# Kernel tuning notes

Hardware: AMD Instinct MI355X
Metric: run time of the kernel (lower is better)

## Reference

```python
import jax, jax.numpy as jnp
import numpy as np

B, D, U = 8192, 2048, 2048  # batch rows, input dim, units
NB_FACTOR = 3
MASK_DENSITY = 1.0 / 16.0  # butterfly-like sparse factor density


def _glorot_uniform(key, shape):
    fan_in, fan_out = shape[0], shape[-1]
    limit = np.sqrt(6.0 / (fan_in + fan_out)).astype(np.float32)
    return jax.random.uniform(key, shape, jnp.float32, -limit, limit)


def setup_inputs() -> dict:
    key = jax.random.key(0)
    kx, km0, km1, km2, kk0, kk1, kk2, ks = jax.random.split(key, 8)
    x = jax.random.normal(kx, (B, D), jnp.float32)
    # Fixed sparsity patterns (constants, like K.constant sparsity_masks)
    m0 = (jax.random.uniform(km0, (D, U)) < MASK_DENSITY).astype(jnp.float32)
    m1 = (jax.random.uniform(km1, (U, U)) < MASK_DENSITY).astype(jnp.float32)
    m2 = (jax.random.uniform(km2, (U, U)) < MASK_DENSITY).astype(jnp.float32)
    k0 = _glorot_uniform(kk0, (D, U))
    k1 = _glorot_uniform(kk1, (U, U))
    k2 = _glorot_uniform(kk2, (U, U))
    scaling = _glorot_uniform(ks, (1,))  # scaler weight, shape (1,)
    bias = jnp.zeros((U,), jnp.float32)
    return {"x": x, "k0": k0, "k1": k1, "k2": k2,
            "m0": m0, "m1": m1, "m2": m2,
            "scaling": scaling, "bias": bias}


def reference(x, k0, k1, k2, m0, m1, m2, scaling, bias):
    # output = activation(scaling * (x @ (k0*m0) @ (k1*m1) @ (k2*m2)) + bias)
    out = x @ (k0 * m0)          # [B, U]
    out = out @ (k1 * m1)        # [B, U]
    out = out @ (k2 * m2)        # [B, U]
    out = scaling * out + bias   # scale then channels-last bias add
    return jax.nn.relu(out)
```

## Files before the change

kernel.cpp:

```cpp
#include <hip/hip_runtime.h>
#include <hip/hip_bf16.h>


typedef __attribute__((ext_vector_type(8))) short  short8;
typedef __attribute__((ext_vector_type(8))) ushort ushort8v;
typedef __attribute__((ext_vector_type(4))) float  f32x4;

#define KD 2048
#define ND 2048

__device__ __forceinline__ ushort f2b(float f) {
    union { float f; unsigned u; } v; v.f = f;
    unsigned r = v.u + 0x7fffu + ((v.u >> 16) & 1u);
    return (ushort)(r >> 16);
}

__device__ __forceinline__ void gload16(const ushort* g, ushort* l) {
    __builtin_amdgcn_global_load_lds(
        (const __attribute__((address_space(1))) void*)g,
        (__attribute__((address_space(3))) void*)l, 16, 0, 0);
}

__global__ __launch_bounds__(256)
void convx(const float* __restrict__ x, ushort* __restrict__ xb)
{
    const size_t i = (size_t)blockIdx.x * 256 + threadIdx.x;
    const float4* src = reinterpret_cast<const float4*>(x) + i * 2;
    const float4 f0 = src[0], f1 = src[1];
    ushort8v u;
    u[0]=f2b(f0.x); u[1]=f2b(f0.y); u[2]=f2b(f0.z); u[3]=f2b(f0.w);
    u[4]=f2b(f1.x); u[5]=f2b(f1.y); u[6]=f2b(f1.z); u[7]=f2b(f1.w);
    reinterpret_cast<ushort8v*>(xb)[i] = u;
}

__global__ __launch_bounds__(256)
void convT3(const float* __restrict__ k0w, const float* __restrict__ k1w,
            const float* __restrict__ k2w, const float* __restrict__ m0w,
            const float* __restrict__ m1w, const float* __restrict__ m2w,
            ushort* __restrict__ wbT)
{
    const int z = blockIdx.z;
    const float* kw = z == 0 ? k0w : (z == 1 ? k1w : k2w);
    const float* mw = z == 0 ? m0w : (z == 1 ? m1w : m2w);
    ushort* o = wbT + (size_t)z * KD * ND;

    __shared__ ushort t[32][36];
    const int tid = threadIdx.x;
    const int bk = blockIdx.x * 32, bn = blockIdx.y * 32;
    {
        const int r = tid >> 3, c = (tid & 7) * 4;
        const size_t g = (size_t)(bk + r) * ND + bn + c;
        const float4 kv = *reinterpret_cast<const float4*>(kw + g);
        const float4 mv = *reinterpret_cast<const float4*>(mw + g);
        t[r][c + 0] = f2b(kv.x * mv.x);
        t[r][c + 1] = f2b(kv.y * mv.y);
        t[r][c + 2] = f2b(kv.z * mv.z);
        t[r][c + 3] = f2b(kv.w * mv.w);
    }
    __syncthreads();
    {
        const int n = tid >> 3, kq = (tid & 7) * 4;
        ushort4 ov;
        ov.x = t[kq + 0][n]; ov.y = t[kq + 1][n];
        ov.z = t[kq + 2][n]; ov.w = t[kq + 3][n];
        *reinterpret_cast<ushort4*>(&o[(size_t)(bn + n) * KD + bk + kq]) = ov;
    }
}

template<int EPI>
__global__ __launch_bounds__(512, 2)
void gemm256(const ushort* __restrict__ A, const ushort* __restrict__ BT,
             void* __restrict__ Cout,
             const float* __restrict__ scaling, const float* __restrict__ bias)
{
    __shared__ ushort S[2][2][2][256 * 32];

    const int tid  = threadIdx.x;
    const int lane = tid & 63;
    const int wid  = tid >> 6;
    const int wr   = wid >> 2, wc = wid & 3;
    const int l15  = lane & 15;
    const int kq   = lane >> 4;
    const int id   = blockIdx.x;
    const int swz  = (id & 7) * 32 + (id >> 3);
    const int bn   = (swz & 7) * 256;
    const int bm   = (swz >> 3) * 256;
    const int srow = lane >> 2;
    const int wrow = wid * 32;
    const int ssw  = ((lane & 3) ^ ((srow >> 1) & 3)) * 8;
    const int rsw  = (kq ^ ((l15 >> 1) & 3)) * 8;

    f32x4 acc[8][4] = {};

#define STAGE(op, bufl, kh, tile, G, g0) do {                                        \
    gload16(G + (size_t)((g0) + wrow + srow)      * KD + (tile)*64 + (kh)*32 + ssw,  \
            &S[bufl][op][kh][(wrow)      * 32]);                                     \
    gload16(G + (size_t)((g0) + wrow + 16 + srow) * KD + (tile)*64 + (kh)*32 + ssw,  \
            &S[bufl][op][kh][(wrow + 16) * 32]);                                     \
  } while (0)

#define BAR()  asm volatile("s_barrier" ::: "memory")
#define VM4()  asm volatile("s_waitcnt vmcnt(4)" ::: "memory")
#define VM0()  asm volatile("s_waitcnt vmcnt(0)" ::: "memory")
#define LGK0() asm volatile("s_waitcnt lgkmcnt(0)" ::: "memory")
#define SB()   __builtin_amdgcn_sched_barrier(0)
#define PRI1() __builtin_amdgcn_s_setprio(1)
#define PRI0() __builtin_amdgcn_s_setprio(0)

#define FA(bufl, kh, m) (*(const short8*)&S[bufl][0][kh][(wr*128 + (m)*16 + l15)*32 + rsw])
#define FB(bufl, kh, n) (*(const short8*)&S[bufl][1][kh][(wc*64  + (n)*16 + l15)*32 + rsw])

#define MF(a_, b_, c_) __builtin_amdgcn_mfma_f32_16x16x32_bf16(a_, b_, c_, 0, 0, 0)

#define MMROW(m, am)                                     \
    acc[m][0] = MF(bf0, am, acc[m][0]);                  \
    acc[m][1] = MF(bf1, am, acc[m][1]);                  \
    acc[m][2] = MF(bf2, am, acc[m][2]);                  \
    acc[m][3] = MF(bf3, am, acc[m][3])

#define PH(bufl, kh, STG, GATE) do {                                                  \
    short8 bf0 = FB(bufl,kh,0);                                                       \
    short8 af0 = FA(bufl,kh,0);                                                       \
    short8 bf1 = FB(bufl,kh,1), bf2 = FB(bufl,kh,2), bf3 = FB(bufl,kh,3);             \
    short8 af1 = FA(bufl,kh,1), af2 = FA(bufl,kh,2), af3 = FA(bufl,kh,3),             \
           af4 = FA(bufl,kh,4), af5 = FA(bufl,kh,5), af6 = FA(bufl,kh,6),             \
           af7 = FA(bufl,kh,7);                                                       \
    STG;                                                                              \
    PRI1();                                                                           \
    MMROW(0, af0); MMROW(1, af1); MMROW(2, af2); MMROW(3, af3);                       \
    MMROW(4, af4); MMROW(5, af5); MMROW(6, af6); MMROW(7, af7);                       \
    PRI0(); SB(); LGK0(); GATE; BAR();                                                \
  } while (0)

    STAGE(0, 0, 0, 0, A,  bm); STAGE(1, 0, 0, 0, BT, bn);
    STAGE(0, 0, 1, 0, A,  bm); STAGE(1, 0, 1, 0, BT, bn);
    STAGE(1, 1, 0, 1, BT, bn); STAGE(0, 1, 0, 1, A,  bm);
    VM4();
    BAR();

    const int NITER = KD / 128;
    for (int it = 0; it < NITER - 1; ++it) {
        const int t1 = 2 * it + 1, t2 = 2 * it + 2, t3 = 2 * it + 3;
        PH(0, 0, STAGE(1,1,1,t1,BT,bn); STAGE(0,1,1,t1,A,bm), );
        PH(0, 1, STAGE(1,0,0,t2,BT,bn); STAGE(0,0,0,t2,A,bm), VM4());
        PH(1, 0, STAGE(1,0,1,t2,BT,bn); STAGE(0,0,1,t2,A,bm), );
        PH(1, 1, STAGE(1,1,0,t3,BT,bn); STAGE(0,1,0,t3,A,bm), VM4());
    }
    PH(0, 0, STAGE(1,1,1,31,BT,bn); STAGE(0,1,1,31,A,bm), );
    PH(0, 1, , VM0());
    PH(1, 0, , );
    PH(1, 1, , );

    const float sc = EPI ? scaling[0] : 0.f;
#pragma unroll
    for (int m = 0; m < 8; ++m) {
        const size_t grow = (size_t)(bm + wr * 128 + m * 16 + l15);
#pragma unroll
        for (int n = 0; n < 4; ++n) {
            const int gcol = bn + wc * 64 + n * 16 + kq * 4;
            if constexpr (EPI) {
                const float4 bv = *reinterpret_cast<const float4*>(bias + gcol);
                float4 v;
                v.x = fmaxf(fmaf(sc, acc[m][n][0], bv.x), 0.f);
                v.y = fmaxf(fmaf(sc, acc[m][n][1], bv.y), 0.f);
                v.z = fmaxf(fmaf(sc, acc[m][n][2], bv.z), 0.f);
                v.w = fmaxf(fmaf(sc, acc[m][n][3], bv.w), 0.f);
                *reinterpret_cast<float4*>((float*)Cout + grow * ND + gcol) = v;
            } else {
                ushort4 v;
                v.x = f2b(acc[m][n][0]); v.y = f2b(acc[m][n][1]);
                v.z = f2b(acc[m][n][2]); v.w = f2b(acc[m][n][3]);
                *reinterpret_cast<ushort4*>((ushort*)Cout + grow * ND + gcol) = v;
            }
        }
    }
#undef STAGE
#undef PH
#undef MF
#undef MMROW
#undef FA
#undef FB
}

extern "C" void kernel_launch(void* const* d_in, const int* in_sizes, int n_in,
                              void* d_out, int out_size, void* d_ws, size_t ws_size,
                              hipStream_t stream)
{
    const float* x    = (const float*)d_in[0];
    const float* k0w  = (const float*)d_in[1];
    const float* k1w  = (const float*)d_in[2];
    const float* k2w  = (const float*)d_in[3];
    const float* m0w  = (const float*)d_in[4];
    const float* m1w  = (const float*)d_in[5];
    const float* m2w  = (const float*)d_in[6];
    const float* sc   = (const float*)d_in[7];
    const float* bias = (const float*)d_in[8];

    const int Md = in_sizes[0] / KD;
    const size_t NE = (size_t)Md * KD;

    ushort* act1 = (ushort*)d_out;
    ushort* xb   = (ushort*)d_out + NE;
    float*  out  = (float*)d_out;
    ushort* act2 = (ushort*)d_ws;
    ushort* wbT  = (ushort*)d_ws + NE;

    dim3 bl(256);
    dim3 gX(NE / (256 * 8));
    dim3 gT(KD / 32, ND / 32, 3);
    dim3 gG((ND / 256) * (Md / 256)), bG(512);

    convx <<<gX, bl, 0, stream>>>(x, xb);
    convT3<<<gT, bl, 0, stream>>>(k0w, k1w, k2w, m0w, m1w, m2w, wbT);

    gemm256<0><<<gG, bG, 0, stream>>>(xb,   wbT,                     act1, nullptr, nullptr);
    gemm256<0><<<gG, bG, 0, stream>>>(act1, wbT + (size_t)KD * ND,     act2, nullptr, nullptr);
    gemm256<1><<<gG, bG, 0, stream>>>(act2, wbT + (size_t)2 * KD * ND, out,  sc, bias);
}
```

Before: 211.9 us.

## Software-pipeline LDS fragment reads one phase ahead of MFMA compute

Adds two register sets for the A and B fragments. Each phase now issues LDS reads for the next half-tile while running MFMAs on fragments loaded in the previous phase, with a prologue read and a trailing MMALL. The aim is to hide LDS read latency behind matrix math instead of stalling before each MFMA burst. In exchange it roughly doubles fragment register use, which may cut occupancy or cause spills, and it changes the vmcnt gating to VM4 on every phase, which could be unsafe.

```diff
diff --git a/kernel.cpp b/kernel.cpp
--- a/kernel.cpp
+++ b/kernel.cpp
@@ -91,6 +91,8 @@
     const int rsw  = (kq ^ ((l15 >> 1) & 3)) * 8;
 
     f32x4 acc[8][4] = {};
+    short8 xa0, xa1, xa2, xa3, xa4, xa5, xa6, xa7, ya0, ya1, ya2, ya3;
+    short8 xb0, xb1, xb2, xb3, xb4, xb5, xb6, xb7, yb0, yb1, yb2, yb3;
 
 #define STAGE(op, bufl, kh, tile, G, g0) do {                                        \
     gload16(G + (size_t)((g0) + wrow + srow)      * KD + (tile)*64 + (kh)*32 + ssw,  \
@@ -112,24 +114,29 @@
 
 #define MF(a_, b_, c_) __builtin_amdgcn_mfma_f32_16x16x32_bf16(a_, b_, c_, 0, 0, 0)
 
-#define MMROW(m, am)                                     \
-    acc[m][0] = MF(bf0, am, acc[m][0]);                  \
-    acc[m][1] = MF(bf1, am, acc[m][1]);                  \
-    acc[m][2] = MF(bf2, am, acc[m][2]);                  \
-    acc[m][3] = MF(bf3, am, acc[m][3])
-
-#define PH(bufl, kh, STG, GATE) do {                                                  \
-    short8 bf0 = FB(bufl,kh,0);                                                       \
-    short8 af0 = FA(bufl,kh,0);                                                       \
-    short8 bf1 = FB(bufl,kh,1), bf2 = FB(bufl,kh,2), bf3 = FB(bufl,kh,3);             \
-    short8 af1 = FA(bufl,kh,1), af2 = FA(bufl,kh,2), af3 = FA(bufl,kh,3),             \
-           af4 = FA(bufl,kh,4), af5 = FA(bufl,kh,5), af6 = FA(bufl,kh,6),             \
-           af7 = FA(bufl,kh,7);                                                       \
-    STG;                                                                              \
-    PRI1();                                                                           \
-    MMROW(0, af0); MMROW(1, af1); MMROW(2, af2); MMROW(3, af3);                       \
-    MMROW(4, af4); MMROW(5, af5); MMROW(6, af6); MMROW(7, af7);                       \
-    PRI0(); SB(); LGK0(); GATE; BAR();                                                \
+#define READS(X, Y, bufl, kh)                                                         \
+    Y##0 = FB(bufl,kh,0); Y##1 = FB(bufl,kh,1);                                       \
+    Y##2 = FB(bufl,kh,2); Y##3 = FB(bufl,kh,3);                                       \
+    X##0 = FA(bufl,kh,0); X##1 = FA(bufl,kh,1);                                       \
+    X##2 = FA(bufl,kh,2); X##3 = FA(bufl,kh,3);                                       \
+    X##4 = FA(bufl,kh,4); X##5 = FA(bufl,kh,5);                                       \
+    X##6 = FA(bufl,kh,6); X##7 = FA(bufl,kh,7);
+
+#define MMROW(m, xm, Y)                                                               \
+    acc[m][0] = MF(Y##0, xm, acc[m][0]);                                              \
+    acc[m][1] = MF(Y##1, xm, acc[m][1]);                                              \
+    acc[m][2] = MF(Y##2, xm, acc[m][2]);                                              \
+    acc[m][3] = MF(Y##3, xm, acc[m][3]);
+
+#define MMALL(X, Y)                                                                   \
+    MMROW(0, X##0, Y) MMROW(1, X##1, Y) MMROW(2, X##2, Y) MMROW(3, X##3, Y)           \
+    MMROW(4, X##4, Y) MMROW(5, X##5, Y) MMROW(6, X##6, Y) MMROW(7, X##7, Y)
+
+#define PH(LX, LY, lbuf, lkh, STG, CX, CY, GATE) do {                                 \
+    READS(LX, LY, lbuf, lkh);                                                         \
+    STG; SB();                                                                        \
+    PRI1(); MMALL(CX, CY); PRI0(); SB();                                              \
+    LGK0(); GATE; BAR();                                                              \
   } while (0)
 
     STAGE(0, 0, 0, 0, A,  bm); STAGE(1, 0, 0, 0, BT, bn);
@@ -137,19 +144,19 @@
     STAGE(1, 1, 0, 1, BT, bn); STAGE(0, 1, 0, 1, A,  bm);
     VM4();
     BAR();
-
-    const int NITER = KD / 128;
-    for (int it = 0; it < NITER - 1; ++it) {
+    READS(xa, ya, 0, 0);
+
+    for (int it = 0; it < 15; ++it) {
         const int t1 = 2 * it + 1, t2 = 2 * it + 2, t3 = 2 * it + 3;
-        PH(0, 0, STAGE(1,1,1,t1,BT,bn); STAGE(0,1,1,t1,A,bm), );
-        PH(0, 1, STAGE(1,0,0,t2,BT,bn); STAGE(0,0,0,t2,A,bm), VM4());
-        PH(1, 0, STAGE(1,0,1,t2,BT,bn); STAGE(0,0,1,t2,A,bm), );
-        PH(1, 1, STAGE(1,1,0,t3,BT,bn); STAGE(0,1,0,t3,A,bm), VM4());
-    }
-    PH(0, 0, STAGE(1,1,1,31,BT,bn); STAGE(0,1,1,31,A,bm), );
-    PH(0, 1, , VM0());
-    PH(1, 0, , );
-    PH(1, 1, , );
+        PH(xb, yb, 0, 1, STAGE(1,1,1,t1,BT,bn); STAGE(0,1,1,t1,A,bm), xa, ya, VM4());
+        PH(xa, ya, 1, 0, STAGE(1,0,0,t2,BT,bn); STAGE(0,0,0,t2,A,bm), xb, yb, VM4());
+        PH(xb, yb, 1, 1, STAGE(1,0,1,t2,BT,bn); STAGE(0,0,1,t2,A,bm), xa, ya, VM4());
+        PH(xa, ya, 0, 0, STAGE(1,1,0,t3,BT,bn); STAGE(0,1,0,t3,A,bm), xb, yb, VM4());
+    }
+    PH(xb, yb, 0, 1, STAGE(1,1,1,31,BT,bn); STAGE(0,1,1,31,A,bm), xa, ya, VM4());
+    PH(xa, ya, 1, 0, , xb, yb, VM0());
+    PH(xb, yb, 1, 1, , xa, ya, );
+    PRI1(); MMALL(xb, yb); PRI0();
 
     const float sc = EPI ? scaling[0] : 0.f;
 #pragma unroll
@@ -178,6 +185,8 @@
 #undef PH
 #undef MF
 #undef MMROW
+#undef MMALL
+#undef READS
 #undef FA
 #undef FB
 }
```

Result: slower. 273.6 us (+29.1%).

## Shrink GEMM block tile to 256x128 with four waves and simple double buffer

Applied to the files above, without the earlier changes.

Changes the GEMM from 256x256 tiles with 8 waves to 256x128 tiles with 4 waves, doubling the grid size. It also replaces the two-stage K=64 interleaved prefetch with a plain double-buffered K=32 loop. That loop waits for all outstanding loads and barriers every step. The aim is more blocks per CU and a simpler schedule, at the cost of less operand reuse per block and more exposed global-load latency.

```diff
diff --git a/kernel.cpp b/kernel.cpp
--- a/kernel.cpp
+++ b/kernel.cpp
@@ -68,47 +68,56 @@
 }
 
 template<int EPI>
-__global__ __launch_bounds__(512, 2)
+__global__ __launch_bounds__(256, 2)
 void gemm256(const ushort* __restrict__ A, const ushort* __restrict__ BT,
              void* __restrict__ Cout,
              const float* __restrict__ scaling, const float* __restrict__ bias)
 {
-    __shared__ ushort S[2][2][2][256 * 32];
+    __shared__ ushort SA[2][256 * 32];
+    __shared__ ushort SB[2][128 * 32];
 
     const int tid  = threadIdx.x;
     const int lane = tid & 63;
     const int wid  = tid >> 6;
-    const int wr   = wid >> 2, wc = wid & 3;
+    const int wr   = wid >> 1, wc = wid & 1;
     const int l15  = lane & 15;
     const int kq   = lane >> 4;
     const int id   = blockIdx.x;
-    const int swz  = (id & 7) * 32 + (id >> 3);
-    const int bn   = (swz & 7) * 256;
-    const int bm   = (swz >> 3) * 256;
+    const int swz  = (id & 7) * 64 + (id >> 3);
+    const int bn   = (swz & 15) * 128;
+    const int bm   = (swz >> 4) * 256;
     const int srow = lane >> 2;
-    const int wrow = wid * 32;
     const int ssw  = ((lane & 3) ^ ((srow >> 1) & 3)) * 8;
     const int rsw  = (kq ^ ((l15 >> 1) & 3)) * 8;
 
     f32x4 acc[8][4] = {};
 
-#define STAGE(op, bufl, kh, tile, G, g0) do {                                        \
-    gload16(G + (size_t)((g0) + wrow + srow)      * KD + (tile)*64 + (kh)*32 + ssw,  \
-            &S[bufl][op][kh][(wrow)      * 32]);                                     \
-    gload16(G + (size_t)((g0) + wrow + 16 + srow) * KD + (tile)*64 + (kh)*32 + ssw,  \
-            &S[bufl][op][kh][(wrow + 16) * 32]);                                     \
+#define STAGE_A(bufl, tile) do {                                                     \
+    gload16(A + (size_t)(bm + wid*64 +  0 + srow) * KD + (tile)*32 + ssw,            \
+            &SA[bufl][(wid*64 +  0) * 32]);                                          \
+    gload16(A + (size_t)(bm + wid*64 + 16 + srow) * KD + (tile)*32 + ssw,            \
+            &SA[bufl][(wid*64 + 16) * 32]);                                          \
+    gload16(A + (size_t)(bm + wid*64 + 32 + srow) * KD + (tile)*32 + ssw,            \
+            &SA[bufl][(wid*64 + 32) * 32]);                                          \
+    gload16(A + (size_t)(bm + wid*64 + 48 + srow) * KD + (tile)*32 + ssw,            \
+            &SA[bufl][(wid*64 + 48) * 32]);                                          \
   } while (0)
+#define STAGE_B(bufl, tile) do {                                                     \
+    gload16(BT + (size_t)(bn + wid*32 +  0 + srow) * KD + (tile)*32 + ssw,           \
+            &SB[bufl][(wid*32 +  0) * 32]);                                          \
+    gload16(BT + (size_t)(bn + wid*32 + 16 + srow) * KD + (tile)*32 + ssw,           \
+            &SB[bufl][(wid*32 + 16) * 32]);                                          \
+  } while (0)
 
 #define BAR()  asm volatile("s_barrier" ::: "memory")
-#define VM4()  asm volatile("s_waitcnt vmcnt(4)" ::: "memory")
 #define VM0()  asm volatile("s_waitcnt vmcnt(0)" ::: "memory")
 #define LGK0() asm volatile("s_waitcnt lgkmcnt(0)" ::: "memory")
-#define SB()   __builtin_amdgcn_sched_barrier(0)
+#define SB_()  __builtin_amdgcn_sched_barrier(0)
 #define PRI1() __builtin_amdgcn_s_setprio(1)
 #define PRI0() __builtin_amdgcn_s_setprio(0)
 
-#define FA(bufl, kh, m) (*(const short8*)&S[bufl][0][kh][(wr*128 + (m)*16 + l15)*32 + rsw])
-#define FB(bufl, kh, n) (*(const short8*)&S[bufl][1][kh][(wc*64  + (n)*16 + l15)*32 + rsw])
+#define FA(bufl, m) (*(const short8*)&SA[bufl][(wr*128 + (m)*16 + l15)*32 + rsw])
+#define FB(bufl, n) (*(const short8*)&SB[bufl][(wc*64  + (n)*16 + l15)*32 + rsw])
 
 #define MF(a_, b_, c_) __builtin_amdgcn_mfma_f32_16x16x32_bf16(a_, b_, c_, 0, 0, 0)
 
@@ -118,38 +127,31 @@
     acc[m][2] = MF(bf2, am, acc[m][2]);                  \
     acc[m][3] = MF(bf3, am, acc[m][3])
 
-#define PH(bufl, kh, STG, GATE) do {                                                  \
-    short8 bf0 = FB(bufl,kh,0);                                                       \
-    short8 af0 = FA(bufl,kh,0);                                                       \
-    short8 bf1 = FB(bufl,kh,1), bf2 = FB(bufl,kh,2), bf3 = FB(bufl,kh,3);             \
-    short8 af1 = FA(bufl,kh,1), af2 = FA(bufl,kh,2), af3 = FA(bufl,kh,3),             \
-           af4 = FA(bufl,kh,4), af5 = FA(bufl,kh,5), af6 = FA(bufl,kh,6),             \
-           af7 = FA(bufl,kh,7);                                                       \
+#define PH(bufl, STG, GATE) do {                                                      \
+    short8 bf0 = FB(bufl,0);                                                          \
+    short8 af0 = FA(bufl,0);                                                          \
+    short8 bf1 = FB(bufl,1), bf2 = FB(bufl,2), bf3 = FB(bufl,3);                      \
+    short8 af1 = FA(bufl,1), af2 = FA(bufl,2), af3 = FA(bufl,3),                      \
+           af4 = FA(bufl,4), af5 = FA(bufl,5), af6 = FA(bufl,6),                      \
+           af7 = FA(bufl,7);                                                          \
     STG;                                                                              \
     PRI1();                                                                           \
     MMROW(0, af0); MMROW(1, af1); MMROW(2, af2); MMROW(3, af3);                       \
     MMROW(4, af4); MMROW(5, af5); MMROW(6, af6); MMROW(7, af7);                       \
-    PRI0(); SB(); LGK0(); GATE; BAR();                                                \
+    PRI0(); SB_(); GATE;                                                              \
   } while (0)
 
-    STAGE(0, 0, 0, 0, A,  bm); STAGE(1, 0, 0, 0, BT, bn);
-    STAGE(0, 0, 1, 0, A,  bm); STAGE(1, 0, 1, 0, BT, bn);
-    STAGE(1, 1, 0, 1, BT, bn); STAGE(0, 1, 0, 1, A,  bm);
-    VM4();
+    STAGE_A(0, 0); STAGE_B(0, 0);
+    VM0();
     BAR();
 
-    const int NITER = KD / 128;
-    for (int it = 0; it < NITER - 1; ++it) {
-        const int t1 = 2 * it + 1, t2 = 2 * it + 2, t3 = 2 * it + 3;
-        PH(0, 0, STAGE(1,1,1,t1,BT,bn); STAGE(0,1,1,t1,A,bm), );
-        PH(0, 1, STAGE(1,0,0,t2,BT,bn); STAGE(0,0,0,t2,A,bm), VM4());
-        PH(1, 0, STAGE(1,0,1,t2,BT,bn); STAGE(0,0,1,t2,A,bm), );
-        PH(1, 1, STAGE(1,1,0,t3,BT,bn); STAGE(0,1,0,t3,A,bm), VM4());
-    }
-    PH(0, 0, STAGE(1,1,1,31,BT,bn); STAGE(0,1,1,31,A,bm), );
-    PH(0, 1, , VM0());
-    PH(1, 0, , );
-    PH(1, 1, , );
+    const int NT = KD / 32;
+    for (int t = 0; t < NT - 1; ++t) {
+        const int bf = t & 1;
+        PH(bf, STAGE_A(bf ^ 1, t + 1); STAGE_B(bf ^ 1, t + 1),
+           LGK0(); VM0(); BAR());
+    }
+    PH(1, , );
 
     const float sc = EPI ? scaling[0] : 0.f;
 #pragma unroll
@@ -174,7 +176,8 @@
             }
         }
     }
-#undef STAGE
+#undef STAGE_A
+#undef STAGE_B
 #undef PH
 #undef MF
 #undef MMROW
@@ -208,7 +211,7 @@
     dim3 bl(256);
     dim3 gX(NE / (256 * 8));
     dim3 gT(KD / 32, ND / 32, 3);
-    dim3 gG((ND / 256) * (Md / 256)), bG(512);
+    dim3 gG((ND / 128) * (Md / 256)), bG(256);
 
     convx <<<gX, bl, 0, stream>>>(x, xb);
     convT3<<<gT, bl, 0, stream>>>(k0w, k1w, k2w, m0w, m1w, m2w, wbT);
```

Result: slower. 239.0 us (+12.8%).
